# Optimization experiments

Hardware: AMD Instinct MI355X
Metric: run time of the kernel (lower is better)

## Reference

```python
import jax, jax.numpy as jnp
import numpy as np

B, DIM, HID = 16384, 1024, 64


def setup_inputs() -> dict:
    key = jax.random.key(0)
    k = jax.random.split(key, 6)
    s1 = 1.0 / np.sqrt(2 * DIM)
    s2 = 1.0 / np.sqrt(HID)
    return {
        "q": jax.random.normal(k[0], (B, DIM), jnp.float32),
        "p": jax.random.normal(k[1], (B, DIM), jnp.float32),
        "W1": jax.random.uniform(k[2], (2 * DIM, HID), jnp.float32, -s1, s1),
        "b1": jax.random.uniform(k[3], (HID,), jnp.float32, -s1, s1),
        "W2": jax.random.uniform(k[4], (HID, DIM), jnp.float32, -s2, s2),
        "b2": jax.random.uniform(k[5], (DIM,), jnp.float32, -s2, s2),
        "mass": jnp.ones((DIM,), jnp.float32),
        "dt_param": jnp.float32(0.1),
    }


def _hamiltonian(qp, W1, b1, W2, b2):
    # torch nn.GELU() default is exact (erf) gelu
    h = jax.nn.gelu(qp @ W1 + b1, approximate=False)
    return h @ W2 + b2  # [B, dim]


def reference(q, p, W1, b1, W2, b2, mass, dt_param):
    dim = q.shape[-1]

    def H_sum(qp):
        return _hamiltonian(qp, W1, b1, W2, b2).sum()

    grad_H = jax.grad(H_sum)

    qp = jnp.concatenate([q, p], axis=-1)  # [B, 2*dim]
    g = grad_H(qp)
    dH_dq = g[:, :dim]

    dt = jax.nn.sigmoid(dt_param)
    p_half = p - dt / 2 * dH_dq
    q_new = q + dt / mass[None, :] * p_half

    qp_new = jnp.concatenate([q_new, p_half], axis=-1)
    g2 = grad_H(qp_new)
    dH_dq_new = g2[:, :dim]
    p_new = p_half - dt / 2 * dH_dq_new

    energy_conserved = jnp.abs(
        _hamiltonian(qp, W1, b1, W2, b2)
        - _hamiltonian(jnp.concatenate([q_new, p_new], axis=-1), W1, b1, W2, b2)
    )  # [B, dim]
    return q_new, p_new, energy_conserved
```

## Files before the change

kernel.cpp:

```cpp
#include <hip/hip_runtime.h>
#include <stdint.h>

#define BROWS 16384
#define DIMN 1024
#define HIDN 64

typedef __attribute__((ext_vector_type(8))) short bf16x8;
typedef __attribute__((ext_vector_type(4))) float f32x4;

__device__ __forceinline__ unsigned short f2bf(float f) {
    union { float f; unsigned int u; } v; v.f = f;
    unsigned int u = v.u;
    u += 0x7fffu + ((u >> 16) & 1u);
    return (unsigned short)(u >> 16);
}

__device__ __forceinline__ bf16x8 pack8(float4 a, float4 b) {
    bf16x8 r;
    r[0] = (short)f2bf(a.x); r[1] = (short)f2bf(a.y);
    r[2] = (short)f2bf(a.z); r[3] = (short)f2bf(a.w);
    r[4] = (short)f2bf(b.x); r[5] = (short)f2bf(b.y);
    r[6] = (short)f2bf(b.z); r[7] = (short)f2bf(b.w);
    return r;
}

__device__ __forceinline__ float geluf(float x) {
    return 0.5f * x * (1.0f + erff(x * 0.70710678118654752f));
}
__device__ __forceinline__ float dgeluf(float x) {
    float c = 0.5f * (1.0f + erff(x * 0.70710678118654752f));
    return c + x * 0.3989422804014327f * expf(-0.5f * x * x);
}


__global__ void w2sum_kernel(const float* __restrict__ W2, float* __restrict__ w2sum) {
    __shared__ float part[4][64];
    int k = threadIdx.x & 63, c = threadIdx.x >> 6;
    float s = 0.f;
    const float* row = W2 + (size_t)k * DIMN + c * 256;
    for (int j = 0; j < 256; ++j) s += row[j];
    part[c][k] = s;
    __syncthreads();
    if (c == 0) w2sum[k] = part[0][k] + part[1][k] + part[2][k] + part[3][k];
}

__global__ void prep_kernel(const float* __restrict__ W1, const float* __restrict__ W2,
                            const float* __restrict__ mass, const float* __restrict__ dtp,
                            unsigned short* __restrict__ W1bf,
                            unsigned short* __restrict__ W1Tbf,
                            unsigned short* __restrict__ W2Tbf,
                            unsigned short* __restrict__ W1qdT,
                            float* __restrict__ dtm) {
    int gid = blockIdx.x * blockDim.x + threadIdx.x;
    int nt = gridDim.x * blockDim.x;
    float dt = 1.0f / (1.0f + expf(-dtp[0]));
    for (int i = gid; i < 2048 * 64; i += nt) {
        unsigned short b = f2bf(W1[i]);
        W1bf[i] = b;
        int k = i >> 6, n = i & 63;
        W1Tbf[n * 2048 + k] = b;
    }
    for (int i = gid; i < 64 * 1024; i += nt) {
        int k = i >> 10, n = i & 1023;
        W2Tbf[n * 64 + k] = f2bf(W2[i]);
    }
    for (int i = gid; i < 64 * 1024; i += nt) {
        int n = i >> 10, k = i & 1023;
        W1qdT[i] = f2bf((dt / mass[k]) * W1[k * 64 + n]);
    }
    for (int i = gid; i < DIMN; i += nt) dtm[i] = dt / mass[i];
}


__global__ __launch_bounds__(256)
void mnkern(const unsigned short* __restrict__ W1T, const unsigned short* __restrict__ W1qdT,
            float* __restrict__ MN, float* __restrict__ Nm) {
    const int wv = threadIdx.x >> 6, lane = threadIdx.x & 63;
    const int l16 = lane & 15, quad = lane >> 4, kq = quad * 8;
    const int gw = blockIdx.x * 4 + wv;
    const int mt = gw >> 2, nt = gw & 3;
    f32x4 accMd = {0,0,0,0}, accN = {0,0,0,0};
    #pragma unroll 4
    for (int it = 0; it < 32; ++it) {
        int k = it * 32 + kq;
        bf16x8 af = *(const bf16x8*)(W1T + (size_t)(mt * 16 + l16) * 2048 + k);
        bf16x8 bd = *(const bf16x8*)(W1qdT + (size_t)(nt * 16 + l16) * 1024 + k);
        bf16x8 bp = *(const bf16x8*)(W1T + (size_t)(nt * 16 + l16) * 2048 + 1024 + k);
        accMd = __builtin_amdgcn_mfma_f32_16x16x32_bf16(af, bd, accMd, 0, 0, 0);
        accN  = __builtin_amdgcn_mfma_f32_16x16x32_bf16(af, bp, accN, 0, 0, 0);
    }
    #pragma unroll
    for (int rg = 0; rg < 4; ++rg) {
        int row = mt * 16 + quad * 4 + rg;
        int col = nt * 16 + l16;
        MN[row * 64 + col] = accMd[rg] + accN[rg];
        Nm[row * 64 + col] = accN[rg];
    }
}


__global__ __launch_bounds__(256, 4)
void zdual(const float* __restrict__ q, const float* __restrict__ p,
           const unsigned short* __restrict__ W1T, const unsigned short* __restrict__ W1qdT,
           const float* __restrict__ b1,
           float* __restrict__ z1g, float* __restrict__ zdpg) {
    __shared__ float part[4 * 64 * 34];
    const int wv = threadIdx.x >> 6, lane = threadIdx.x & 63;
    const int l16 = lane & 15, quad = lane >> 4, kq = quad * 8;
    const int tile = blockIdx.x;
    const size_t arow = (size_t)tile * 16 + l16;
    const float* rq = q + arow * DIMN;
    const float* rp = p + arow * DIMN;
    const int k0 = wv * 256;

    f32x4 accz[4] = {{0,0,0,0},{0,0,0,0},{0,0,0,0},{0,0,0,0}};
    f32x4 accd[4] = {{0,0,0,0},{0,0,0,0},{0,0,0,0},{0,0,0,0}};

    #pragma unroll 4
    for (int it = 0; it < 8; ++it) {
        int k = k0 + it * 32 + kq;
        float4 a0 = *(const float4*)(rq + k);
        float4 a1 = *(const float4*)(rq + k + 4);
        bf16x8 af = pack8(a0, a1);
        #pragma unroll
        for (int c = 0; c < 4; ++c) {
            bf16x8 bf = *(const bf16x8*)(W1T + (size_t)(c * 16 + l16) * 2048 + k);
            accz[c] = __builtin_amdgcn_mfma_f32_16x16x32_bf16(af, bf, accz[c], 0, 0, 0);
        }
    }
    #pragma unroll 2
    for (int it = 0; it < 8; ++it) {
        int k = k0 + it * 32 + kq;
        float4 a0 = *(const float4*)(rp + k);
        float4 a1 = *(const float4*)(rp + k + 4);
        bf16x8 af = pack8(a0, a1);
        #pragma unroll
        for (int c = 0; c < 4; ++c) {
            bf16x8 bfp = *(const bf16x8*)(W1T + (size_t)(c * 16 + l16) * 2048 + 1024 + k);
            accz[c] = __builtin_amdgcn_mfma_f32_16x16x32_bf16(af, bfp, accz[c], 0, 0, 0);
            bf16x8 bfd = *(const bf16x8*)(W1qdT + (size_t)(c * 16 + l16) * 1024 + k);
            accd[c] = __builtin_amdgcn_mfma_f32_16x16x32_bf16(af, bfd, accd[c], 0, 0, 0);
        }
    }

    float* myp = part + (size_t)(wv * 64 + lane) * 34;
    #pragma unroll
    for (int c = 0; c < 4; ++c) {
        #pragma unroll
        for (int rg = 0; rg < 4; ++rg) {
            myp[c * 4 + rg] = accz[c][rg];
            myp[16 + c * 4 + rg] = accd[c][rg];
        }
    }
    __syncthreads();
    for (int e = threadIdx.x; e < 1024; e += 256) {
        int row = e >> 6, col = e & 63;
        int ln = ((row >> 2) << 4) | (col & 15);
        int j = ((col >> 4) << 2) | (row & 3);
        float sz = b1[col], sd = 0.f;
        #pragma unroll
        for (int w = 0; w < 4; ++w) {
            const float* pp = part + (size_t)(w * 64 + ln) * 34;
            sz += pp[j];
            sd += pp[16 + j];
        }
        size_t o = ((size_t)tile * 16 + row) * 64 + col;
        z1g[o] = sz;
        zdpg[o] = sd;
    }
}


__global__ __launch_bounds__(256, 4)
void chain(const float* __restrict__ z1g, const float* __restrict__ zdpg,
           const float* __restrict__ MN, const float* __restrict__ Nm,
           const float* __restrict__ w2sum, const float* __restrict__ dtp,
           unsigned short* __restrict__ u1b, unsigned short* __restrict__ usb,
           unsigned short* __restrict__ g13) {
    __shared__ float ubuf[4 * 256];
    const int wv = threadIdx.x >> 6, lane = threadIdx.x & 63;
    float* ub = ubuf + wv * 256;
    const int r0 = (blockIdx.x * 4 + wv) * 4;
    const float ws = w2sum[lane];
    const float hdt = 0.5f / (1.0f + expf(-dtp[0]));

    float z1v[4], zdv[4], u1[4], h1[4];
    #pragma unroll
    for (int r = 0; r < 4; ++r) {
        z1v[r] = z1g[(size_t)(r0 + r) * 64 + lane];
        zdv[r] = zdpg[(size_t)(r0 + r) * 64 + lane];
        u1[r] = dgeluf(z1v[r]) * ws;
        h1[r] = geluf(z1v[r]);
        ub[r * 64 + lane] = u1[r];
    }
    float acc[4] = {0.f, 0.f, 0.f, 0.f};
    #pragma unroll 8
    for (int k = 0; k < 64; ++k) {
        float m = MN[k * 64 + lane];
        acc[0] += ub[k] * m;
        acc[1] += ub[64 + k] * m;
        acc[2] += ub[128 + k] * m;
        acc[3] += ub[192 + k] * m;
    }
    float z2[4], u2[4];
    #pragma unroll
    for (int r = 0; r < 4; ++r) {
        z2[r] = z1v[r] + zdv[r] - hdt * acc[r];
        u2[r] = dgeluf(z2[r]) * ws;
        ub[r * 64 + lane] = u2[r];
    }
    float acc2[4] = {0.f, 0.f, 0.f, 0.f};
    #pragma unroll 8
    for (int k = 0; k < 64; ++k) {
        float m = Nm[k * 64 + lane];
        acc2[0] += ub[k] * m;
        acc2[1] += ub[64 + k] * m;
        acc2[2] += ub[128 + k] * m;
        acc2[3] += ub[192 + k] * m;
    }
    #pragma unroll
    for (int r = 0; r < 4; ++r) {
        float z3 = z2[r] - hdt * acc2[r];
        size_t o = (size_t)(r0 + r) * 64 + lane;
        u1b[o] = f2bf(u1[r]);
        usb[o] = f2bf(u1[r] + u2[r]);
        g13[o] = f2bf(h1[r] - geluf(z3));
    }
}


__global__ __launch_bounds__(256, 4)
void widefused(const unsigned short* __restrict__ u1b, const unsigned short* __restrict__ usb,
               const unsigned short* __restrict__ g13,
               const unsigned short* __restrict__ W1bf, const unsigned short* __restrict__ W2T,
               const float* __restrict__ q, const float* __restrict__ p,
               const float* __restrict__ dtm, const float* __restrict__ dtp,
               float* __restrict__ outq, float* __restrict__ outp, float* __restrict__ oute) {
    const int wv = threadIdx.x >> 6, lane = threadIdx.x & 63;
    const int l16 = lane & 15, quad = lane >> 4, kq = quad * 8;
    const int gw = blockIdx.x * 4 + wv;
    const int mt = gw >> 6, nt = gw & 63;
    const size_t arow = (size_t)mt * 16 + l16;
    const int n0 = nt * 16;

    bf16x8 au0 = *(const bf16x8*)(u1b + arow * 64 + kq);
    bf16x8 au1 = *(const bf16x8*)(u1b + arow * 64 + 32 + kq);
    bf16x8 as0 = *(const bf16x8*)(usb + arow * 64 + kq);
    bf16x8 as1 = *(const bf16x8*)(usb + arow * 64 + 32 + kq);
    bf16x8 ag0 = *(const bf16x8*)(g13 + arow * 64 + kq);
    bf16x8 ag1 = *(const bf16x8*)(g13 + arow * 64 + 32 + kq);
    bf16x8 bw0 = *(const bf16x8*)(W1bf + (size_t)(n0 + l16) * 64 + kq);
    bf16x8 bw1 = *(const bf16x8*)(W1bf + (size_t)(n0 + l16) * 64 + 32 + kq);
    bf16x8 b20 = *(const bf16x8*)(W2T + (size_t)(n0 + l16) * 64 + kq);
    bf16x8 b21 = *(const bf16x8*)(W2T + (size_t)(n0 + l16) * 64 + 32 + kq);

    f32x4 accq = {0,0,0,0}, accs = {0,0,0,0}, acce = {0,0,0,0};
    accq = __builtin_amdgcn_mfma_f32_16x16x32_bf16(au0, bw0, accq, 0, 0, 0);
    accq = __builtin_amdgcn_mfma_f32_16x16x32_bf16(au1, bw1, accq, 0, 0, 0);
    accs = __builtin_amdgcn_mfma_f32_16x16x32_bf16(as0, bw0, accs, 0, 0, 0);
    accs = __builtin_amdgcn_mfma_f32_16x16x32_bf16(as1, bw1, accs, 0, 0, 0);
    acce = __builtin_amdgcn_mfma_f32_16x16x32_bf16(ag0, b20, acce, 0, 0, 0);
    acce = __builtin_amdgcn_mfma_f32_16x16x32_bf16(ag1, b21, acce, 0, 0, 0);

    const int i = n0 + l16;
    const float hdt = 0.5f / (1.0f + expf(-dtp[0]));
    const float dm = dtm[i];
    #pragma unroll
    for (int rg = 0; rg < 4; ++rg) {
        size_t idx = (size_t)(mt * 16 + quad * 4 + rg) * DIMN + i;
        float qv = q[idx], pv = p[idx];
        float ph = pv - hdt * accq[rg];
        outq[idx] = qv + dm * ph;
        outp[idx] = pv - hdt * accs[rg];
        oute[idx] = fabsf(acce[rg]);
    }
}


extern "C" void kernel_launch(void* const* d_in, const int* in_sizes, int n_in,
                              void* d_out, int out_size, void* d_ws, size_t ws_size,
                              hipStream_t stream) {
    const float* q    = (const float*)d_in[0];
    const float* p    = (const float*)d_in[1];
    const float* W1   = (const float*)d_in[2];
    const float* b1   = (const float*)d_in[3];
    const float* W2   = (const float*)d_in[4];
    const float* mass = (const float*)d_in[6];
    const float* dtp  = (const float*)d_in[7];

    float* out  = (float*)d_out;
    float* outq = out;
    float* outp = out + (size_t)BROWS * DIMN;
    float* oute = out + (size_t)2 * BROWS * DIMN;

    char* ws = (char*)d_ws;
    unsigned short* W1bf  = (unsigned short*)(ws);
    unsigned short* W1Tbf = (unsigned short*)(ws + 262144);
    unsigned short* W2Tbf = (unsigned short*)(ws + 524288);
    float* w2sum          = (float*)(ws + 655360);
    float* dtm            = (float*)(ws + 655616);
    unsigned short* W1qdT = (unsigned short*)(ws + 659712);
    float* MN             = (float*)(ws + 790784);
    float* Nm             = (float*)(ws + 807168);
    float* z1             = (float*)(ws + 1048576);
    float* zdp            = (float*)(ws + 5242880);
    unsigned short* u1b   = (unsigned short*)(ws + 9437184);
    unsigned short* usb   = (unsigned short*)(ws + 11534336);
    unsigned short* g13   = (unsigned short*)(ws + 13631488);

    hipLaunchKernelGGL(w2sum_kernel, dim3(1), dim3(256), 0, stream, W2, w2sum);
    hipLaunchKernelGGL(prep_kernel, dim3(256), dim3(256), 0, stream,
                       W1, W2, mass, dtp, W1bf, W1Tbf, W2Tbf, W1qdT, dtm);
    hipLaunchKernelGGL(mnkern, dim3(4), dim3(256), 0, stream, W1Tbf, W1qdT, MN, Nm);
    hipLaunchKernelGGL(zdual, dim3(1024), dim3(256), 0, stream,
                       q, p, W1Tbf, W1qdT, b1, z1, zdp);
    hipLaunchKernelGGL(chain, dim3(1024), dim3(256), 0, stream,
                       z1, zdp, MN, Nm, w2sum, dtp, u1b, usb, g13);
    hipLaunchKernelGGL(widefused, dim3(16384), dim3(256), 0, stream,
                       u1b, usb, g13, W1bf, W2Tbf, q, p, dtm, dtp, outq, outp, oute);
}
```

Before: 455.4 us.

## Fuse zdual into chain, merge w2sum into prep, prefetch loads, widen output tiles

The z-projection kernel and the per-row chain kernel become one kernel, so the z1/zdp intermediates stay on-chip and never round-trip through global memory. The W2 row-sum moves into block 0 of the prep kernel, which drops one launch. The q/p GEMM loop now software-prefetches the next slice and handles q and p in a single pass. The final kernel gives each wave four N-tiles, reusing its A fragments and launching a quarter as many blocks. The costs are higher register pressure in the fused kernel and less parallelism in the last stage.

```diff
diff --git a/kernel.cpp b/kernel.cpp
--- a/kernel.cpp
+++ b/kernel.cpp
@@ -33,24 +33,24 @@
 }
 
 
-__global__ void w2sum_kernel(const float* __restrict__ W2, float* __restrict__ w2sum) {
-    __shared__ float part[4][64];
-    int k = threadIdx.x & 63, c = threadIdx.x >> 6;
-    float s = 0.f;
-    const float* row = W2 + (size_t)k * DIMN + c * 256;
-    for (int j = 0; j < 256; ++j) s += row[j];
-    part[c][k] = s;
-    __syncthreads();
-    if (c == 0) w2sum[k] = part[0][k] + part[1][k] + part[2][k] + part[3][k];
-}
-
 __global__ void prep_kernel(const float* __restrict__ W1, const float* __restrict__ W2,
                             const float* __restrict__ mass, const float* __restrict__ dtp,
                             unsigned short* __restrict__ W1bf,
                             unsigned short* __restrict__ W1Tbf,
                             unsigned short* __restrict__ W2Tbf,
                             unsigned short* __restrict__ W1qdT,
-                            float* __restrict__ dtm) {
+                            float* __restrict__ dtm, float* __restrict__ w2sum) {
+    if (blockIdx.x == 0) {
+        __shared__ float partw[4][64];
+        int k = threadIdx.x & 63, c = threadIdx.x >> 6;
+        float s = 0.f;
+        const float* row = W2 + (size_t)k * DIMN + c * 256;
+        #pragma unroll 8
+        for (int j = 0; j < 256; ++j) s += row[j];
+        partw[c][k] = s;
+        __syncthreads();
+        if (c == 0) w2sum[k] = partw[0][k] + partw[1][k] + partw[2][k] + partw[3][k];
+    }
     int gid = blockIdx.x * blockDim.x + threadIdx.x;
     int nt = gridDim.x * blockDim.x;
     float dt = 1.0f / (1.0f + expf(-dtp[0]));
@@ -100,47 +100,53 @@
 
 
 __global__ __launch_bounds__(256, 4)
-void zdual(const float* __restrict__ q, const float* __restrict__ p,
-           const unsigned short* __restrict__ W1T, const unsigned short* __restrict__ W1qdT,
-           const float* __restrict__ b1,
-           float* __restrict__ z1g, float* __restrict__ zdpg) {
+void zchain(const float* __restrict__ q, const float* __restrict__ p,
+            const unsigned short* __restrict__ W1T, const unsigned short* __restrict__ W1qdT,
+            const float* __restrict__ b1,
+            const float* __restrict__ MN, const float* __restrict__ Nm,
+            const float* __restrict__ w2sum, const float* __restrict__ dtp,
+            unsigned short* __restrict__ u1b, unsigned short* __restrict__ usb,
+            unsigned short* __restrict__ g13) {
     __shared__ float part[4 * 64 * 34];
+    __shared__ float ubuf[4 * 256];
     const int wv = threadIdx.x >> 6, lane = threadIdx.x & 63;
     const int l16 = lane & 15, quad = lane >> 4, kq = quad * 8;
     const int tile = blockIdx.x;
     const size_t arow = (size_t)tile * 16 + l16;
-    const float* rq = q + arow * DIMN;
-    const float* rp = p + arow * DIMN;
-    const int k0 = wv * 256;
+    const float* rq = q + arow * DIMN + wv * 256;
+    const float* rp = p + arow * DIMN + wv * 256;
 
     f32x4 accz[4] = {{0,0,0,0},{0,0,0,0},{0,0,0,0},{0,0,0,0}};
     f32x4 accd[4] = {{0,0,0,0},{0,0,0,0},{0,0,0,0},{0,0,0,0}};
 
-    #pragma unroll 4
+    float4 cq0 = *(const float4*)(rq + kq);
+    float4 cq1 = *(const float4*)(rq + kq + 4);
+    float4 cp0 = *(const float4*)(rp + kq);
+    float4 cp1 = *(const float4*)(rp + kq + 4);
+    #pragma unroll
     for (int it = 0; it < 8; ++it) {
-        int k = k0 + it * 32 + kq;
-        float4 a0 = *(const float4*)(rq + k);
-        float4 a1 = *(const float4*)(rq + k + 4);
-        bf16x8 af = pack8(a0, a1);
+        float4 nq0 = {0,0,0,0}, nq1 = {0,0,0,0}, np0 = {0,0,0,0}, np1 = {0,0,0,0};
+        if (it < 7) {
+            int kn = (it + 1) * 32 + kq;
+            nq0 = *(const float4*)(rq + kn); nq1 = *(const float4*)(rq + kn + 4);
+            np0 = *(const float4*)(rp + kn); np1 = *(const float4*)(rp + kn + 4);
+        }
+        const int k = wv * 256 + it * 32 + kq;
+        bf16x8 aq = pack8(cq0, cq1);
+        bf16x8 ap = pack8(cp0, cp1);
         #pragma unroll
         for (int c = 0; c < 4; ++c) {
-            bf16x8 bf = *(const bf16x8*)(W1T + (size_t)(c * 16 + l16) * 2048 + k);
-            accz[c] = __builtin_amdgcn_mfma_f32_16x16x32_bf16(af, bf, accz[c], 0, 0, 0);
-        }
-    }
-    #pragma unroll 2
-    for (int it = 0; it < 8; ++it) {
-        int k = k0 + it * 32 + kq;
-        float4 a0 = *(const float4*)(rp + k);
-        float4 a1 = *(const float4*)(rp + k + 4);
-        bf16x8 af = pack8(a0, a1);
+            bf16x8 bq = *(const bf16x8*)(W1T + (size_t)(c * 16 + l16) * 2048 + k);
+            accz[c] = __builtin_amdgcn_mfma_f32_16x16x32_bf16(aq, bq, accz[c], 0, 0, 0);
+        }
         #pragma unroll
         for (int c = 0; c < 4; ++c) {
-            bf16x8 bfp = *(const bf16x8*)(W1T + (size_t)(c * 16 + l16) * 2048 + 1024 + k);
-            accz[c] = __builtin_amdgcn_mfma_f32_16x16x32_bf16(af, bfp, accz[c], 0, 0, 0);
-            bf16x8 bfd = *(const bf16x8*)(W1qdT + (size_t)(c * 16 + l16) * 1024 + k);
-            accd[c] = __builtin_amdgcn_mfma_f32_16x16x32_bf16(af, bfd, accd[c], 0, 0, 0);
-        }
+            bf16x8 bp = *(const bf16x8*)(W1T + (size_t)(c * 16 + l16) * 2048 + 1024 + k);
+            accz[c] = __builtin_amdgcn_mfma_f32_16x16x32_bf16(ap, bp, accz[c], 0, 0, 0);
+            bf16x8 bd = *(const bf16x8*)(W1qdT + (size_t)(c * 16 + l16) * 1024 + k);
+            accd[c] = __builtin_amdgcn_mfma_f32_16x16x32_bf16(ap, bd, accd[c], 0, 0, 0);
+        }
+        cq0 = nq0; cq1 = nq1; cp0 = np0; cp1 = np1;
     }
 
     float* myp = part + (size_t)(wv * 64 + lane) * 34;
@@ -153,10 +159,13 @@
         }
     }
     __syncthreads();
-    for (int e = threadIdx.x; e < 1024; e += 256) {
-        int row = e >> 6, col = e & 63;
-        int ln = ((row >> 2) << 4) | (col & 15);
-        int j = ((col >> 4) << 2) | (row & 3);
+
+    float z1v[4], zdv[4];
+    #pragma unroll
+    for (int kk = 0; kk < 4; ++kk) {
+        const int row = wv + kk * 4, col = lane;
+        const int ln = ((row >> 2) << 4) | (col & 15);
+        const int j = ((col >> 4) << 2) | (row & 3);
         float sz = b1[col], sd = 0.f;
         #pragma unroll
         for (int w = 0; w < 4; ++w) {
@@ -164,31 +173,17 @@
             sz += pp[j];
             sd += pp[16 + j];
         }
-        size_t o = ((size_t)tile * 16 + row) * 64 + col;
-        z1g[o] = sz;
-        zdpg[o] = sd;
-    }
-}
-
-
-__global__ __launch_bounds__(256, 4)
-void chain(const float* __restrict__ z1g, const float* __restrict__ zdpg,
-           const float* __restrict__ MN, const float* __restrict__ Nm,
-           const float* __restrict__ w2sum, const float* __restrict__ dtp,
-           unsigned short* __restrict__ u1b, unsigned short* __restrict__ usb,
-           unsigned short* __restrict__ g13) {
-    __shared__ float ubuf[4 * 256];
-    const int wv = threadIdx.x >> 6, lane = threadIdx.x & 63;
+        z1v[kk] = sz;
+        zdv[kk] = sd;
+    }
+
     float* ub = ubuf + wv * 256;
-    const int r0 = (blockIdx.x * 4 + wv) * 4;
     const float ws = w2sum[lane];
     const float hdt = 0.5f / (1.0f + expf(-dtp[0]));
 
-    float z1v[4], zdv[4], u1[4], h1[4];
+    float u1[4], h1[4];
     #pragma unroll
     for (int r = 0; r < 4; ++r) {
-        z1v[r] = z1g[(size_t)(r0 + r) * 64 + lane];
-        zdv[r] = zdpg[(size_t)(r0 + r) * 64 + lane];
         u1[r] = dgeluf(z1v[r]) * ws;
         h1[r] = geluf(z1v[r]);
         ub[r * 64 + lane] = u1[r];
@@ -221,7 +216,7 @@
     #pragma unroll
     for (int r = 0; r < 4; ++r) {
         float z3 = z2[r] - hdt * acc2[r];
-        size_t o = (size_t)(r0 + r) * 64 + lane;
+        size_t o = ((size_t)tile * 16 + wv + r * 4) * 64 + lane;
         u1b[o] = f2bf(u1[r]);
         usb[o] = f2bf(u1[r] + u2[r]);
         g13[o] = f2bf(h1[r] - geluf(z3));
@@ -230,18 +225,18 @@
 
 
 __global__ __launch_bounds__(256, 4)
-void widefused(const unsigned short* __restrict__ u1b, const unsigned short* __restrict__ usb,
-               const unsigned short* __restrict__ g13,
-               const unsigned short* __restrict__ W1bf, const unsigned short* __restrict__ W2T,
-               const float* __restrict__ q, const float* __restrict__ p,
-               const float* __restrict__ dtm, const float* __restrict__ dtp,
-               float* __restrict__ outq, float* __restrict__ outp, float* __restrict__ oute) {
+void wide4(const unsigned short* __restrict__ u1b, const unsigned short* __restrict__ usb,
+           const unsigned short* __restrict__ g13,
+           const unsigned short* __restrict__ W1bf, const unsigned short* __restrict__ W2T,
+           const float* __restrict__ q, const float* __restrict__ p,
+           const float* __restrict__ dtm, const float* __restrict__ dtp,
+           float* __restrict__ outq, float* __restrict__ outp, float* __restrict__ oute) {
     const int wv = threadIdx.x >> 6, lane = threadIdx.x & 63;
     const int l16 = lane & 15, quad = lane >> 4, kq = quad * 8;
     const int gw = blockIdx.x * 4 + wv;
-    const int mt = gw >> 6, nt = gw & 63;
+    const int mt = gw >> 4;
+    const int ng = (gw & 15) * 4;
     const size_t arow = (size_t)mt * 16 + l16;
-    const int n0 = nt * 16;
 
     bf16x8 au0 = *(const bf16x8*)(u1b + arow * 64 + kq);
     bf16x8 au1 = *(const bf16x8*)(u1b + arow * 64 + 32 + kq);
@@ -249,30 +244,36 @@
     bf16x8 as1 = *(const bf16x8*)(usb + arow * 64 + 32 + kq);
     bf16x8 ag0 = *(const bf16x8*)(g13 + arow * 64 + kq);
     bf16x8 ag1 = *(const bf16x8*)(g13 + arow * 64 + 32 + kq);
-    bf16x8 bw0 = *(const bf16x8*)(W1bf + (size_t)(n0 + l16) * 64 + kq);
-    bf16x8 bw1 = *(const bf16x8*)(W1bf + (size_t)(n0 + l16) * 64 + 32 + kq);
-    bf16x8 b20 = *(const bf16x8*)(W2T + (size_t)(n0 + l16) * 64 + kq);
-    bf16x8 b21 = *(const bf16x8*)(W2T + (size_t)(n0 + l16) * 64 + 32 + kq);
-
-    f32x4 accq = {0,0,0,0}, accs = {0,0,0,0}, acce = {0,0,0,0};
-    accq = __builtin_amdgcn_mfma_f32_16x16x32_bf16(au0, bw0, accq, 0, 0, 0);
-    accq = __builtin_amdgcn_mfma_f32_16x16x32_bf16(au1, bw1, accq, 0, 0, 0);
-    accs = __builtin_amdgcn_mfma_f32_16x16x32_bf16(as0, bw0, accs, 0, 0, 0);
-    accs = __builtin_amdgcn_mfma_f32_16x16x32_bf16(as1, bw1, accs, 0, 0, 0);
-    acce = __builtin_amdgcn_mfma_f32_16x16x32_bf16(ag0, b20, acce, 0, 0, 0);
-    acce = __builtin_amdgcn_mfma_f32_16x16x32_bf16(ag1, b21, acce, 0, 0, 0);
-
-    const int i = n0 + l16;
+
     const float hdt = 0.5f / (1.0f + expf(-dtp[0]));
-    const float dm = dtm[i];
-    #pragma unroll
-    for (int rg = 0; rg < 4; ++rg) {
-        size_t idx = (size_t)(mt * 16 + quad * 4 + rg) * DIMN + i;
-        float qv = q[idx], pv = p[idx];
-        float ph = pv - hdt * accq[rg];
-        outq[idx] = qv + dm * ph;
-        outp[idx] = pv - hdt * accs[rg];
-        oute[idx] = fabsf(acce[rg]);
+
+    #pragma unroll
+    for (int t = 0; t < 4; ++t) {
+        const int n0 = (ng + t) * 16;
+        bf16x8 bw0 = *(const bf16x8*)(W1bf + (size_t)(n0 + l16) * 64 + kq);
+        bf16x8 bw1 = *(const bf16x8*)(W1bf + (size_t)(n0 + l16) * 64 + 32 + kq);
+        bf16x8 b20 = *(const bf16x8*)(W2T + (size_t)(n0 + l16) * 64 + kq);
+        bf16x8 b21 = *(const bf16x8*)(W2T + (size_t)(n0 + l16) * 64 + 32 + kq);
+
+        f32x4 accq = {0,0,0,0}, accs = {0,0,0,0}, acce = {0,0,0,0};
+        accq = __builtin_amdgcn_mfma_f32_16x16x32_bf16(au0, bw0, accq, 0, 0, 0);
+        accq = __builtin_amdgcn_mfma_f32_16x16x32_bf16(au1, bw1, accq, 0, 0, 0);
+        accs = __builtin_amdgcn_mfma_f32_16x16x32_bf16(as0, bw0, accs, 0, 0, 0);
+        accs = __builtin_amdgcn_mfma_f32_16x16x32_bf16(as1, bw1, accs, 0, 0, 0);
+        acce = __builtin_amdgcn_mfma_f32_16x16x32_bf16(ag0, b20, acce, 0, 0, 0);
+        acce = __builtin_amdgcn_mfma_f32_16x16x32_bf16(ag1, b21, acce, 0, 0, 0);
+
+        const int i = n0 + l16;
+        const float dm = dtm[i];
+        #pragma unroll
+        for (int rg = 0; rg < 4; ++rg) {
+            size_t idx = (size_t)(mt * 16 + quad * 4 + rg) * DIMN + i;
+            float qv = q[idx], pv = p[idx];
+            float ph = pv - hdt * accq[rg];
+            outq[idx] = qv + dm * ph;
+            outp[idx] = pv - hdt * accs[rg];
+            oute[idx] = fabsf(acce[rg]);
+        }
     }
 }
 
@@ -302,20 +303,15 @@
     unsigned short* W1qdT = (unsigned short*)(ws + 659712);
     float* MN             = (float*)(ws + 790784);
     float* Nm             = (float*)(ws + 807168);
-    float* z1             = (float*)(ws + 1048576);
-    float* zdp            = (float*)(ws + 5242880);
     unsigned short* u1b   = (unsigned short*)(ws + 9437184);
     unsigned short* usb   = (unsigned short*)(ws + 11534336);
     unsigned short* g13   = (unsigned short*)(ws + 13631488);
 
-    hipLaunchKernelGGL(w2sum_kernel, dim3(1), dim3(256), 0, stream, W2, w2sum);
     hipLaunchKernelGGL(prep_kernel, dim3(256), dim3(256), 0, stream,
-                       W1, W2, mass, dtp, W1bf, W1Tbf, W2Tbf, W1qdT, dtm);
+                       W1, W2, mass, dtp, W1bf, W1Tbf, W2Tbf, W1qdT, dtm, w2sum);
     hipLaunchKernelGGL(mnkern, dim3(4), dim3(256), 0, stream, W1Tbf, W1qdT, MN, Nm);
-    hipLaunchKernelGGL(zdual, dim3(1024), dim3(256), 0, stream,
-                       q, p, W1Tbf, W1qdT, b1, z1, zdp);
-    hipLaunchKernelGGL(chain, dim3(1024), dim3(256), 0, stream,
-                       z1, zdp, MN, Nm, w2sum, dtp, u1b, usb, g13);
-    hipLaunchKernelGGL(widefused, dim3(16384), dim3(256), 0, stream,
+    hipLaunchKernelGGL(zchain, dim3(1024), dim3(256), 0, stream,
+                       q, p, W1Tbf, W1qdT, b1, MN, Nm, w2sum, dtp, u1b, usb, g13);
+    hipLaunchKernelGGL(wide4, dim3(4096), dim3(256), 0, stream,
                        u1b, usb, g13, W1bf, W2Tbf, q, p, dtm, dtp, outq, outp, oute);
 }
```

Result: faster. 428.5 us (-5.9%).
